# Kernel optimization log

Measured on AMD Instinct MI355X. Metric: run time of the kernel, lower is better.

The kernel has to match this reference:

```python
import jax, jax.numpy as jnp
import numpy as np

N_USERS = 50000
N_ITEMS = 100000
N = N_USERS + N_ITEMS
D = 64
N_LAYERS = 3
N_INTENTS = 128
T_SIZE = 32
TEMP = 0.2
KL_REG = 0.01
EMB_REG = 1e-5
INT_REG = 1e-5
SSL_REG = 0.1
B = 4096
E_RAND = 3_000_000


def setup_inputs() -> dict:
    key = jax.random.key(0)
    ks = jax.random.split(key, 12)
    # edge list: random edges + self loops so every node has degree >= 1
    h_rand = jax.random.randint(ks[0], (E_RAND,), 0, N, dtype=jnp.int32)
    t_rand = jax.random.randint(ks[1], (E_RAND,), 0, N, dtype=jnp.int32)
    loops = jnp.arange(N, dtype=jnp.int32)
    h_list = jnp.concatenate([loops, h_rand])
    t_list = jnp.concatenate([loops, t_rand])
    return {
        "user_emb": jax.random.normal(ks[2], (N_USERS, D), jnp.float32) * 0.1,
        "item_emb": jax.random.normal(ks[3], (N_ITEMS, D), jnp.float32) * 0.1,
        "user_intent": jax.random.normal(ks[4], (D, N_INTENTS), jnp.float32) * 0.1,
        "item_intent": jax.random.normal(ks[5], (D, N_INTENTS), jnp.float32) * 0.1,
        "lin_w": jax.random.normal(ks[6], (D, T_SIZE), jnp.float32) * 0.1,
        "lin_b": jnp.zeros((D,), jnp.float32),
        "eps": jax.random.uniform(ks[7], (N, D), jnp.float32),
        "h_list": h_list,
        "t_list": t_list,
        "users": jax.random.randint(ks[8], (B,), 0, N_USERS, dtype=jnp.int32),
        "pos_items": jax.random.randint(ks[9], (B,), 0, N_ITEMS, dtype=jnp.int32),
        "neg_items": jax.random.randint(ks[10], (B,), 0, N_ITEMS, dtype=jnp.int32),
    }


def _normalize(x):
    return x / jnp.linalg.norm(x, axis=1, keepdims=True)


def _infonce(e1, e2):
    pos = jnp.exp(jnp.sum(e1 * e2, axis=1) / TEMP)                 # [B]
    neg = jnp.sum(jnp.exp(e1 @ e2.T / TEMP), axis=1)               # [B]
    return jnp.mean(-jnp.log(pos / (neg + 1e-8) + 1e-8))


def reference(user_emb, item_emb, user_intent, item_intent, lin_w, lin_b,
              eps, h_list, t_list, users, pos_items, neg_items):
    # ---- symmetric normalization D^-1/2 A D^-1/2 (A values = 1) ----
    deg = jax.ops.segment_sum(jnp.ones_like(h_list, dtype=jnp.float32), h_list,
                              num_segments=N)
    d_inv = deg ** -0.5
    g_vals = d_inv[h_list] * d_inv[t_list]                          # [E]

    # ---- multi-layer SpMM propagation, layer-sum aggregation ----
    ego = jnp.concatenate([user_emb, item_emb], axis=0)             # [N, D]
    acc = ego
    cur = ego
    for _ in range(N_LAYERS):
        cur = jax.ops.segment_sum(g_vals[:, None] * cur[t_list], h_list,
                                  num_segments=N)                   # spmm
        acc = acc + cur
    all_emb = acc                                                   # [N, D]
    ua, ia = all_emb[:N_USERS], all_emb[N_USERS:]

    # ---- generative learning ----
    mean = all_emb
    std = jax.nn.softplus(all_emb[:, :T_SIZE])
    std = std @ lin_w.T + lin_b + 1e-8                              # [N, D]
    gen_emb = mean + eps * std

    # ---- intent model ----
    u_int = jax.nn.softmax(ua @ user_intent, axis=1) @ user_intent.T
    i_int = jax.nn.softmax(ia @ item_intent, axis=1) @ item_intent.T

    # ---- BPR loss ----
    u_e = ua[users]
    pos_scores = jnp.sum(u_e * ia[pos_items], axis=1)
    neg_scores = jnp.sum(u_e * ia[neg_items], axis=1)
    bpr_loss = jnp.mean(jax.nn.softplus(neg_scores - pos_scores))

    # ---- KL loss ----
    kl = -0.5 * (1.0 + 2.0 * std - jnp.square(mean) - jnp.exp(2.0 * std))
    kl = jnp.where(jnp.isfinite(kl), kl, 0.0)
    kl_loss = KL_REG * jnp.mean(jnp.sum(kl, axis=1))
    gen_loss = bpr_loss + kl_loss

    # ---- embedding / intent regularizers ----
    emb_loss = EMB_REG * (jnp.sum(jnp.square(user_emb[users]))
                          + jnp.sum(jnp.square(item_emb[pos_items]))
                          + jnp.sum(jnp.square(item_emb[neg_items])))
    int_loss = INT_REG * (jnp.sum(jnp.square(user_intent))
                          + jnp.sum(jnp.square(item_intent)))

    # ---- SSL (InfoNCE) loss ----
    u_gen = _normalize(gen_emb[:N_USERS][users])
    i_gen = _normalize(gen_emb[N_USERS:][pos_items])
    u_i = _normalize(u_int[users])
    i_i = _normalize(i_int[pos_items])
    cl_loss = SSL_REG * (_infonce(u_gen, u_i) + _infonce(i_gen, i_i))

    return (gen_loss, cl_loss, emb_loss, int_loss)
```

## Files before the change

### kernel.cpp

```cpp
#include <hip/hip_runtime.h>

#define NU 50000
#define NI 100000
#define NT 150000
#define BB 4096
#define NBUCK 147
#define BCAP 24576
#define NCH 8

typedef __attribute__((ext_vector_type(8))) short bf16x8;
typedef __attribute__((ext_vector_type(4))) float f32x4;
typedef __attribute__((ext_vector_type(2))) float f32x2;
typedef unsigned long long u64;

__device__ __forceinline__ float softplusf(float x) {
  return fmaxf(x, 0.f) + __logf(1.f + __expf(-fabsf(x)));
}
__device__ __forceinline__ float wsum(float v) {
#pragma unroll
  for (int o = 32; o > 0; o >>= 1) v += __shfl_xor(v, o, 64);
  return v;
}
__device__ __forceinline__ unsigned short f2b(float x) {
  unsigned u = __float_as_uint(x);
  return (unsigned short)((u + 0x7FFFu + ((u >> 16) & 1u)) >> 16);
}
__device__ __forceinline__ float b2f(unsigned us) {
  return __uint_as_float(us << 16);
}
__device__ __forceinline__ float bfe(bf16x8 v, int j) {
  return __uint_as_float(((unsigned)(unsigned short)v[j]) << 16);
}
__device__ __forceinline__ void unp4(u64 v, float* o) {
  unsigned lo = (unsigned)v, hi = (unsigned)(v >> 32);
  o[0] = __uint_as_float(lo << 16);
  o[1] = __uint_as_float(lo & 0xffff0000u);
  o[2] = __uint_as_float(hi << 16);
  o[3] = __uint_as_float(hi & 0xffff0000u);
}
__device__ __forceinline__ u64 pk4(float x0, float x1, float x2, float x3) {
  return (u64)((unsigned)f2b(x0) | ((unsigned)f2b(x1) << 16)) |
         ((u64)((unsigned)f2b(x2) | ((unsigned)f2b(x3) << 16)) << 32);
}

__global__ void k_zero(int* __restrict__ gcur, float* __restrict__ negu,
                       float* __restrict__ negi, double* __restrict__ accums) {
  int t = threadIdx.x;
  for (int i = t; i < NBUCK; i += 256) gcur[i] = 0;
  for (int i = t; i < BB; i += 256) { negu[i] = 0.f; negi[i] = 0.f; }
  if (t < 8) accums[t] = 0.0;
}

__global__ __launch_bounds__(256) void k_part(const int* __restrict__ h,
                                              const int* __restrict__ t,
                                              int* __restrict__ gcur,
                                              uint2* __restrict__ part, int E) {
  __shared__ int cnt[NBUCK];
  __shared__ int base[NBUCK];
  for (int b = threadIdx.x; b < NBUCK; b += 256) cnt[b] = 0;
  __syncthreads();
  int e0 = blockIdx.x * 4096 + threadIdx.x * 16;
  int nval = E - e0;
  nval = nval < 0 ? 0 : (nval > 16 ? 16 : nval);
  int hh[16], tt[16];
  if (nval == 16) {
    const int4* hp = (const int4*)(h + e0);
    const int4* tp = (const int4*)(t + e0);
#pragma unroll
    for (int j = 0; j < 4; j++) {
      int4 v = hp[j];
      hh[j * 4] = v.x; hh[j * 4 + 1] = v.y; hh[j * 4 + 2] = v.z; hh[j * 4 + 3] = v.w;
      int4 w = tp[j];
      tt[j * 4] = w.x; tt[j * 4 + 1] = w.y; tt[j * 4 + 2] = w.z; tt[j * 4 + 3] = w.w;
    }
  } else {
    for (int j = 0; j < nval; j++) { hh[j] = h[e0 + j]; tt[j] = t[e0 + j]; }
  }
  for (int j = 0; j < nval; j++) atomicAdd(&cnt[hh[j] >> 10], 1);
  __syncthreads();
  for (int b = threadIdx.x; b < NBUCK; b += 256) {
    int c = cnt[b];
    base[b] = c ? atomicAdd(&gcur[b], c) : 0;
    cnt[b] = 0;
  }
  __syncthreads();
  for (int j = 0; j < nval; j++) {
    int b = hh[j] >> 10;
    int r = atomicAdd(&cnt[b], 1);
    uint2 v; v.x = (unsigned)hh[j]; v.y = (unsigned)tt[j];
    part[(size_t)b * BCAP + base[b] + r] = v;
  }
}

__global__ __launch_bounds__(256) void k_count2(const uint2* __restrict__ part,
                                                const int* __restrict__ gcur,
                                                int* __restrict__ cnt_chunk) {
  __shared__ int hist[1024];
  int b = blockIdx.x, c = blockIdx.y, tid = threadIdx.x;
  for (int i = tid; i < 1024; i += 256) hist[i] = 0;
  __syncthreads();
  int m = gcur[b];
  int lo = (int)(((long long)m * c) >> 3);
  int hi = (int)(((long long)m * (c + 1)) >> 3);
  const uint2* pp = part + (size_t)b * BCAP;
  for (int i = lo + tid; i < hi; i += 256) atomicAdd(&hist[pp[i].x & 1023], 1);
  __syncthreads();
  for (int i = tid; i < 1024; i += 256)
    cnt_chunk[((((size_t)b << 10) + i) << 3) + c] = hist[i];
}

__global__ __launch_bounds__(256) void k_node(int* __restrict__ cnt_chunk,
                                              int* __restrict__ rloc_g,
                                              float* __restrict__ d_inv,
                                              int* __restrict__ btot) {
  __shared__ int sd[256];
  int b = blockIdx.x, tid = threadIdx.x;
  int n0 = b << 10;
  int pd[4];
  int s = 0;
#pragma unroll
  for (int j = 0; j < 4; j++) {
    int idx = tid * 4 + j;
    size_t base = ((size_t)(n0 + idx)) << 3;
    int run = 0;
#pragma unroll
// ... 106 lines not shown
  for (int i = s; i < e; i += 32) {
    int ia = i + (int)d;
    int ib = ia + 16;
    u64 ra = ep[ia < e ? ia : e - 1];
    u64 rb = ep[ib < e ? ib : e - 1];
    unsigned rax = (unsigned)ra;
    unsigned ray = (ia < e) ? (unsigned)(ra >> 32) : 0u;
    unsigned rbx = (unsigned)rb;
    unsigned rby = (ib < e) ? (unsigned)(rb >> 32) : 0u;
    unsigned iA0 = __shfl(rax, b4 + 0, 64); float gA0 = __uint_as_float(__shfl(ray, b4 + 0, 64));
    unsigned iA1 = __shfl(rax, b4 + 1, 64); float gA1 = __uint_as_float(__shfl(ray, b4 + 1, 64));
    unsigned iA2 = __shfl(rax, b4 + 2, 64); float gA2 = __uint_as_float(__shfl(ray, b4 + 2, 64));
    unsigned iA3 = __shfl(rax, b4 + 3, 64); float gA3 = __uint_as_float(__shfl(ray, b4 + 3, 64));
    unsigned vA0 = cur[(iA0 << 4) + d];
    unsigned vA1 = cur[(iA1 << 4) + d];
    unsigned vA2 = cur[(iA2 << 4) + d];
    unsigned vA3 = cur[(iA3 << 4) + d];
    unsigned iB0 = __shfl(rbx, b4 + 0, 64); float gB0 = __uint_as_float(__shfl(rby, b4 + 0, 64));
    unsigned iB1 = __shfl(rbx, b4 + 1, 64); float gB1 = __uint_as_float(__shfl(rby, b4 + 1, 64));
    unsigned iB2 = __shfl(rbx, b4 + 2, 64); float gB2 = __uint_as_float(__shfl(rby, b4 + 2, 64));
    unsigned iB3 = __shfl(rbx, b4 + 3, 64); float gB3 = __uint_as_float(__shfl(rby, b4 + 3, 64));
    unsigned vB0 = cur[(iB0 << 4) + d];
    unsigned vB1 = cur[(iB1 << 4) + d];
    unsigned vB2 = cur[(iB2 << 4) + d];
    unsigned vB3 = cur[(iB3 << 4) + d];
    f32x2 lo, hi;
    lo = __builtin_amdgcn_cvt_pk_f32_fp8(vA0, false);
    hi = __builtin_amdgcn_cvt_pk_f32_fp8(vA0, true);
    a0 = fmaf(gA0, lo.x, a0); a1 = fmaf(gA0, lo.y, a1);
    a2 = fmaf(gA0, hi.x, a2); a3 = fmaf(gA0, hi.y, a3);
    lo = __builtin_amdgcn_cvt_pk_f32_fp8(vA1, false);
    hi = __builtin_amdgcn_cvt_pk_f32_fp8(vA1, true);
    a0 = fmaf(gA1, lo.x, a0); a1 = fmaf(gA1, lo.y, a1);
    a2 = fmaf(gA1, hi.x, a2); a3 = fmaf(gA1, hi.y, a3);
    lo = __builtin_amdgcn_cvt_pk_f32_fp8(vA2, false);
    hi = __builtin_amdgcn_cvt_pk_f32_fp8(vA2, true);
    a0 = fmaf(gA2, lo.x, a0); a1 = fmaf(gA2, lo.y, a1);
    a2 = fmaf(gA2, hi.x, a2); a3 = fmaf(gA2, hi.y, a3);
    lo = __builtin_amdgcn_cvt_pk_f32_fp8(vA3, false);
    hi = __builtin_amdgcn_cvt_pk_f32_fp8(vA3, true);
    a0 = fmaf(gA3, lo.x, a0); a1 = fmaf(gA3, lo.y, a1);
    a2 = fmaf(gA3, hi.x, a2); a3 = fmaf(gA3, hi.y, a3);
    lo = __builtin_amdgcn_cvt_pk_f32_fp8(vB0, false);
    hi = __builtin_amdgcn_cvt_pk_f32_fp8(vB0, true);
    a0 = fmaf(gB0, lo.x, a0); a1 = fmaf(gB0, lo.y, a1);
    a2 = fmaf(gB0, hi.x, a2); a3 = fmaf(gB0, hi.y, a3);
    lo = __builtin_amdgcn_cvt_pk_f32_fp8(vB1, false);
    hi = __builtin_amdgcn_cvt_pk_f32_fp8(vB1, true);
    a0 = fmaf(gB1, lo.x, a0); a1 = fmaf(gB1, lo.y, a1);
    a2 = fmaf(gB1, hi.x, a2); a3 = fmaf(gB1, hi.y, a3);
    lo = __builtin_amdgcn_cvt_pk_f32_fp8(vB2, false);
    hi = __builtin_amdgcn_cvt_pk_f32_fp8(vB2, true);
    a0 = fmaf(gB2, lo.x, a0); a1 = fmaf(gB2, lo.y, a1);
    a2 = fmaf(gB2, hi.x, a2); a3 = fmaf(gB2, hi.y, a3);
    lo = __builtin_amdgcn_cvt_pk_f32_fp8(vB3, false);
    hi = __builtin_amdgcn_cvt_pk_f32_fp8(vB3, true);
    a0 = fmaf(gB3, lo.x, a0); a1 = fmaf(gB3, lo.y, a1);
    a2 = fmaf(gB3, hi.x, a2); a3 = fmaf(gB3, hi.y, a3);
  }
  a0 += __shfl_xor(a0, 16, 64);
  a1 += __shfl_xor(a1, 16, 64);
  a2 += __shfl_xor(a2, 16, 64);
  a3 += __shfl_xor(a3, 16, 64);
  a0 += __shfl_xor(a0, 32, 64);
  a1 += __shfl_xor(a1, 32, 64);
  a2 += __shfl_xor(a2, 32, 64);
  a3 += __shfl_xor(a3, 32, 64);
  unsigned ro = ((unsigned)node << 4) + d;
  if (g == 0) {
    u64 pv = acc64[ro];
    unsigned lo32 = (unsigned)pv, hi32 = (unsigned)(pv >> 32);
    float x0 = __uint_as_float(lo32 << 16) + a0;
    float x1 = __uint_as_float(lo32 & 0xffff0000u) + a1;
    float x2 = __uint_as_float(hi32 << 16) + a2;
    float x3 = __uint_as_float(hi32 & 0xffff0000u) + a3;
    acc64[ro] = pk4(x0, x1, x2, x3);
  } else if (g == 1 && !last) {
    int p = __builtin_amdgcn_cvt_pk_fp8_f32(a0, a1, 0, false);
    p = __builtin_amdgcn_cvt_pk_fp8_f32(a2, a3, p, true);
    nxt[ro] = (unsigned)p;
  }
}

__global__ __launch_bounds__(256) void k_post(
    const unsigned short* __restrict__ accB,
    const float* __restrict__ user_emb, const float* __restrict__ item_emb,
    const float* __restrict__ eps,
    const float* __restrict__ user_int, const float* __restrict__ item_int,
    const float* __restrict__ lin_w, const float* __restrict__ lin_b,
    const int* __restrict__ users, const int* __restrict__ pos_items,
    const int* __restrict__ neg_items,
    unsigned short* __restrict__ ugen_b, unsigned short* __restrict__ uio_b,
    unsigned short* __restrict__ igen_b, unsigned short* __restrict__ iio_b,
    float* __restrict__ posu, float* __restrict__ posi,
    double* __restrict__ accums) {
  __shared__ __align__(16) unsigned short sUIT[128 * 72];
  __shared__ __align__(16) unsigned short sUI[64 * 136];
  __shared__ __align__(16) unsigned short sP[4][16 * 136];
  __shared__ double red[8];
  int bid = blockIdx.x;
  int lane = threadIdx.x & 63;
  int wid = threadIdx.x >> 6;
  int n = lane & 15, q = lane >> 4;
  if (bid < 128) {
    int isI = bid >> 6;
    int i0 = ((bid & 63) << 6) + wid * 16;
    const float* intent = isI ? item_int : user_int;
    for (int i = threadIdx.x; i < 8192; i += 256) {
      int dd = i >> 7, kk = i & 127;
      unsigned short v = f2b(intent[i]);
      sUIT[kk * 72 + dd] = v;
      sUI[dd * 136 + kk] = v;
    }
    __syncthreads();
    unsigned short* myP = &sP[wid][0];
    int piN = pos_items[i0 + n];
    int rw = isI ? (NU + piN) : users[i0 + n];
    const unsigned short* arp = accB + (size_t)rw * 64;
    bf16x8 a0 = *(const bf16x8*)(arp + q * 8);
    bf16x8 a1 = *(const bf16x8*)(arp + 32 + q * 8);
    f32x4 c[8];
#pragma unroll
    for (int kt = 0; kt < 8; kt++) {
      const unsigned short* bp = &sUIT[(kt * 16 + n) * 72 + q * 8];
      bf16x8 b0 = *(const bf16x8*)bp;
      bf16x8 b1 = *(const bf16x8*)(bp + 32);
      f32x4 z = {0.f, 0.f, 0.f, 0.f};
      z = __builtin_amdgcn_mfma_f32_16x16x32_bf16(a0, b0, z, 0, 0, 0);
      c[kt] = __builtin_amdgcn_mfma_f32_16x16x32_bf16(a1, b1, z, 0, 0, 0);
    }
    float mx[4], tot[4];
#pragma unroll
    for (int r = 0; r < 4; r++) {
      float m = c[0][r];
#pragma unroll
      for (int kt = 1; kt < 8; kt++) m = fmaxf(m, c[kt][r]);
#pragma unroll
      for (int o = 1; o < 16; o <<= 1) m = fmaxf(m, __shfl_xor(m, o, 64));
      mx[r] = m;
    }
#pragma unroll
    for (int kt = 0; kt < 8; kt++)
#pragma unroll
      for (int r = 0; r < 4; r++) c[kt][r] = __expf(c[kt][r] - mx[r]);
#pragma unroll
    for (int r = 0; r < 4; r++) {
      float t = 0.f;
#pragma unroll
      for (int kt = 0; kt < 8; kt++) t += c[kt][r];
#pragma unroll
      for (int o = 1; o < 16; o <<= 1) t += __shfl_xor(t, o, 64);
      tot[r] = 1.f / t;
    }
#pragma unroll
    for (int kt = 0; kt < 8; kt++)
#pragma unroll
      for (int r = 0; r < 4; r++)
        myP[(q * 4 + r) * 136 + kt * 16 + n] = f2b(c[kt][r] * tot[r]);
    f32x4 s[4];
#pragma unroll
    for (int dt = 0; dt < 4; dt++) s[dt] = (f32x4){0.f, 0.f, 0.f, 0.f};
#pragma unroll
    for (int cc = 0; cc < 4; cc++) {
      bf16x8 pa = *(const bf16x8*)&myP[n * 136 + cc * 32 + q * 8];
#pragma unroll
      for (int dt = 0; dt < 4; dt++) {
        bf16x8 bb = *(const bf16x8*)&sUI[(dt * 16 + n) * 136 + cc * 32 + q * 8];
        s[dt] = __builtin_amdgcn_mfma_f32_16x16x32_bf16(pa, bb, s[dt], 0, 0, 0);
      }
    }
    float rin[4];
#pragma unroll
    for (int r = 0; r < 4; r++) {
      float t = 0.f;
#pragma unroll
      for (int dt = 0; dt < 4; dt++) t += s[dt][r] * s[dt][r];
#pragma unroll
      for (int o = 1; o < 16; o <<= 1) t += __shfl_xor(t, o, 64);
      rin[r] = 1.f / sqrtf(t);
    }
    float iov[4][4];
    unsigned short* iob = isI ? iio_b : uio_b;
#pragma unroll
    for (int dt = 0; dt < 4; dt++)
#pragma unroll
      for (int r = 0; r < 4; r++) {
        float v = s[dt][r] * rin[r];
        iov[dt][r] = v;
        iob[(size_t)(i0 + q * 4 + r) * 64 + dt * 16 + n] = f2b(v);
      }
    bf16x8 A3;
#pragma unroll
    for (int j = 0; j < 8; j++) A3[j] = (short)f2b(softplusf(bfe(a0, j)));
    f32x4 sd4[4];
    float lbv[4];
#pragma unroll
    for (int dt = 0; dt < 4; dt++) {
      const float* wp = lin_w + (size_t)(dt * 16 + n) * 32 + q * 8;
      float4 w0 = *(const float4*)wp;
      float4 w1 = *(const float4*)(wp + 4);
      bf16x8 B3;
      B3[0] = (short)f2b(w0.x); B3[1] = (short)f2b(w0.y);
      B3[2] = (short)f2b(w0.z); B3[3] = (short)f2b(w0.w);
      B3[4] = (short)f2b(w1.x); B3[5] = (short)f2b(w1.y);
      B3[6] = (short)f2b(w1.z); B3[7] = (short)f2b(w1.w);
      f32x4 z = {0.f, 0.f, 0.f, 0.f};
      sd4[dt] = __builtin_amdgcn_mfma_f32_16x16x32_bf16(A3, B3, z, 0, 0, 0);
      lbv[dt] = lin_b[dt * 16 + n];
    }
    *(bf16x8*)&myP[n * 136 + q * 8] = a0;
    *(bf16x8*)&myP[n * 136 + 32 + q * 8] = a1;
    int rwr[4];
#pragma unroll
    for (int r = 0; r < 4; r++) rwr[r] = __shfl(rw, q * 4 + r, 64);
    float ge[4][4];
#pragma unroll
    for (int dt = 0; dt < 4; dt++)
#pragma unroll
      for (int r = 0; r < 4; r++) {
        float mcv = b2f(myP[(q * 4 + r) * 136 + dt * 16 + n]);
        float ep = eps[(size_t)rwr[r] * 64 + dt * 16 + n];
        float sdf = sd4[dt][r] + lbv[dt] + 1e-8f;
        ge[dt][r] = mcv + ep * sdf;
      }
    float gin[4];
#pragma unroll
    for (int r = 0; r < 4; r++) {
      float t = 0.f;
#pragma unroll
      for (int dt = 0; dt < 4; dt++) t += ge[dt][r] * ge[dt][r];
#pragma unroll
      for (int o = 1; o < 16; o <<= 1) t += __shfl_xor(t, o, 64);
      gin[r] = 1.f / sqrtf(t);
    }
    float pd[4] = {0.f, 0.f, 0.f, 0.f};
    unsigned short* gob = isI ? igen_b : ugen_b;
#pragma unroll
    for (int dt = 0; dt < 4; dt++)
#pragma unroll
      for (int r = 0; r < 4; r++) {
        float go = ge[dt][r] * gin[r];
        gob[(size_t)(i0 + q * 4 + r) * 64 + dt * 16 + n] = f2b(go);
        pd[r] = fmaf(go, iov[dt][r], pd[r]);
      }
    float* posX = isI ? posi : posu;
#pragma unroll
    for (int r = 0; r < 4; r++) {
      float t = pd[r];
#pragma unroll
      for (int o = 1; o < 16; o <<= 1) t += __shfl_xor(t, o, 64);
      if (n == 0) posX[i0 + q * 4 + r] = t;
    }
    if (!isI) {
      int niN = neg_items[i0 + n];
      const unsigned short* pp = accB + (size_t)(NU + piN) * 64;
      const unsigned short* np = accB + (size_t)(NU + niN) * 64;
      bf16x8 p0 = *(const bf16x8*)(pp + q * 8);
      bf16x8 p1 = *(const bf16x8*)(pp + 32 + q * 8);
      bf16x8 n0 = *(const bf16x8*)(np + q * 8);
      bf16x8 n1 = *(const bf16x8*)(np + 32 + q * 8);
      float ps = 0.f, ns = 0.f;
#pragma unroll
      for (int j = 0; j < 8; j++) {
        float m0 = bfe(a0, j), m1 = bfe(a1, j);
        ps = fmaf(m0, bfe(p0, j), ps); ps = fmaf(m1, bfe(p1, j), ps);
        ns = fmaf(m0, bfe(n0, j), ns); ns = fmaf(m1, bfe(n1, j), ns);
      }
      ps += __shfl_xor(ps, 16, 64); ps += __shfl_xor(ps, 32, 64);
      ns += __shfl_xor(ns, 16, 64); ns += __shfl_xor(ns, 32, 64);
      float bpr = softplusf(ns - ps);
      const float* uep = user_emb + (size_t)rw * 64 + q * 16;
      float es = 0.f;
#pragma unroll
      for (int j = 0; j < 4; j++) {
        float4 u4 = *(const float4*)(uep + j * 4);
        es += u4.x * u4.x + u4.y * u4.y + u4.z * u4.z + u4.w * u4.w;
      }
      es += __shfl_xor(es, 16, 64); es += __shfl_xor(es, 32, 64);
#pragma unroll
      for (int o = 1; o < 16; o <<= 1) {
        bpr += __shfl_xor(bpr, o, 64);
        es += __shfl_xor(es, o, 64);
      }
      if (lane == 0) { red[wid] = (double)bpr; red[4 + wid] = (double)es; }
      __syncthreads();
      if (threadIdx.x == 0) {
        atomicAdd(&accums[0], red[0] + red[1] + red[2] + red[3]);
        atomicAdd(&accums[2], red[4] + red[5] + red[6] + red[7]);
      }
    } else {
      int niN = neg_items[i0 + n];
      const float* pe = item_emb + (size_t)piN * 64 + q * 16;
      const float* ne = item_emb + (size_t)niN * 64 + q * 16;
      float es = 0.f;
#pragma unroll
      for (int j = 0; j < 4; j++) {
        float4 u4 = *(const float4*)(pe + j * 4);
        float4 v4 = *(const float4*)(ne + j * 4);
        es += u4.x * u4.x + u4.y * u4.y + u4.z * u4.z + u4.w * u4.w;
        es += v4.x * v4.x + v4.y * v4.y + v4.z * v4.z + v4.w * v4.w;
      }
      es += __shfl_xor(es, 16, 64); es += __shfl_xor(es, 32, 64);
#pragma unroll
      for (int o = 1; o < 16; o <<= 1) es += __shfl_xor(es, o, 64);
      if (lane == 0) red[wid] = (double)es;
      __syncthreads();
      if (threadIdx.x == 0)
        atomicAdd(&accums[2], red[0] + red[1] + red[2] + red[3]);
    }
  } else if (bid < 128 + 1920) {
    bf16x8 B0, B1, B2, B3;
    float lb0, lb1, lb2, lb3;
    {
      const float* w0 = lin_w + (0 * 16 + n) * 32 + q * 8;
      const float* w1 = lin_w + (1 * 16 + n) * 32 + q * 8;
      const float* w2 = lin_w + (2 * 16 + n) * 32 + q * 8;
      const float* w3 = lin_w + (3 * 16 + n) * 32 + q * 8;
#pragma unroll
      for (int j = 0; j < 8; j++) {
        B0[j] = (short)f2b(w0[j]);
        B1[j] = (short)f2b(w1[j]);
        B2[j] = (short)f2b(w2[j]);
        B3[j] = (short)f2b(w3[j]);
      }
      lb0 = lin_b[0 * 16 + n] + 1e-8f;
      lb1 = lin_b[1 * 16 + n] + 1e-8f;
      lb2 = lin_b[2 * 16 + n] + 1e-8f;
      lb3 = lin_b[3 * 16 + n] + 1e-8f;
    }
    const int TI = NT / 16;
    int w0id = (bid - 128) * 4 + wid;
    int nwv = 1920 * 4;
    double dsum = 0.0;
    for (int tile = w0id; tile < TI; tile += nwv) {
      const u64* rp = (const u64*)(accB + (size_t)(tile * 16 + n) * 64 + q * 8);
      u64 A0 = rp[0];
      u64 A1 = rp[1];
      u64 C0 = rp[8];
      u64 C1 = rp[9];
      float av[8], bv[8];
      unp4(A0, av); unp4(A1, av + 4);
      unp4(C0, bv); unp4(C1, bv + 4);
      float msum = 0.f;
#pragma unroll
      for (int j = 0; j < 8; j++) msum += av[j] * av[j] + bv[j] * bv[j];
      bf16x8 Af;
#pragma unroll
      for (int j = 0; j < 8; j++) Af[j] = (short)f2b(softplusf(av[j]));
      f32x4 z = {0.f, 0.f, 0.f, 0.f};
      f32x4 c0 = __builtin_amdgcn_mfma_f32_16x16x32_bf16(Af, B0, z, 0, 0, 0);
      f32x4 c1 = __builtin_amdgcn_mfma_f32_16x16x32_bf16(Af, B1, z, 0, 0, 0);
      f32x4 c2 = __builtin_amdgcn_mfma_f32_16x16x32_bf16(Af, B2, z, 0, 0, 0);
      f32x4 c3 = __builtin_amdgcn_mfma_f32_16x16x32_bf16(Af, B3, z, 0, 0, 0);
      float ksum = 0.f;
#pragma unroll
      for (int r = 0; r < 4; r++) {
        float s0 = c0[r] + lb0, s1 = c1[r] + lb1, s2 = c2[r] + lb2, s3 = c3[r] + lb3;
        ksum += -0.5f * (1.f + 2.f * s0 - __expf(2.f * s0));
        ksum += -0.5f * (1.f + 2.f * s1 - __expf(2.f * s1));
        ksum += -0.5f * (1.f + 2.f * s2 - __expf(2.f * s2));
        ksum += -0.5f * (1.f + 2.f * s3 - __expf(2.f * s3));
      }
      dsum += (double)wsum(ksum + 0.5f * msum);
    }
    if (lane == 0) red[wid] = dsum;
    __syncthreads();
    if (threadIdx.x == 0)
      atomicAdd(&accums[1], red[0] + red[1] + red[2] + red[3]);
  } else {
    float s = 0.f;
    for (int i = threadIdx.x; i < 64 * 128; i += 256) {
      float a = user_int[i], b = item_int[i];
      s = fmaf(a, a, s);
      s = fmaf(b, b, s);
    }
    s = wsum(s);
    if (lane == 0) red[wid] = (double)s;
    __syncthreads();
    if (threadIdx.x == 0)
      atomicAdd(&accums[3], red[0] + red[1] + red[2] + red[3]);
  }
}

__global__ __launch_bounds__(256) void k_nce(
    const unsigned short* __restrict__ e1u, const unsigned short* __restrict__ e2u,
    const unsigned short* __restrict__ e1i, const unsigned short* __restrict__ e2i,
    float* __restrict__ negu, float* __restrict__ negi) {
  int pr = blockIdx.y >> 4, jq = blockIdx.y & 15;
  const unsigned short* e1 = pr ? e1i : e1u;
  const unsigned short* e2 = pr ? e2i : e2u;
  float* nego = pr ? negi : negu;
  int wid = threadIdx.x >> 6, lane = threadIdx.x & 63;
  int q = lane >> 4, n = lane & 15;
  int i0 = blockIdx.x * 64 + wid * 16;
  const bf16x8* arow = (const bf16x8*)(e1 + (size_t)(i0 + n) * 64 + q * 8);
  bf16x8 a0 = arow[0];
  bf16x8 a1 = arow[4];
  f32x4 accv = {0.f, 0.f, 0.f, 0.f};
  int j0 = jq * 256;
  for (int jt = 0; jt < 16; jt += 2) {
    const bf16x8* br0 = (const bf16x8*)(e2 + (size_t)(j0 + jt * 16 + n) * 64 + q * 8);
    const bf16x8* br1 = (const bf16x8*)(e2 + (size_t)(j0 + (jt + 1) * 16 + n) * 64 + q * 8);
    bf16x8 b0 = br0[0];
    bf16x8 b1 = br0[4];
    bf16x8 b2 = br1[0];
    bf16x8 b3 = br1[4];
    f32x4 c = {0.f, 0.f, 0.f, 0.f};
    f32x4 c2 = {0.f, 0.f, 0.f, 0.f};
    c = __builtin_amdgcn_mfma_f32_16x16x32_bf16(a0, b0, c, 0, 0, 0);
    c = __builtin_amdgcn_mfma_f32_16x16x32_bf16(a1, b1, c, 0, 0, 0);
    c2 = __builtin_amdgcn_mfma_f32_16x16x32_bf16(a0, b2, c2, 0, 0, 0);
    c2 = __builtin_amdgcn_mfma_f32_16x16x32_bf16(a1, b3, c2, 0, 0, 0);
#pragma unroll
    for (int r = 0; r < 4; r++)
      accv[r] += __expf(5.0f * c[r]) + __expf(5.0f * c2[r]);
  }
#pragma unroll
  for (int o = 1; o < 16; o <<= 1) {
#pragma unroll
    for (int r = 0; r < 4; r++) accv[r] += __shfl_xor(accv[r], o, 64);
  }
  if (n == 0) {
#pragma unroll
    for (int r = 0; r < 4; r++) atomicAdd(&nego[i0 + q * 4 + r], accv[r]);
  }
}

__global__ __launch_bounds__(256) void k_out(
    const float* __restrict__ posu, const float* __restrict__ posi,
    const float* __restrict__ negu, const float* __restrict__ negi,
    const double* __restrict__ accums, float* __restrict__ out) {
  __shared__ double redd[4];
  double cl = 0.0;
  for (int i = threadIdx.x; i < 2 * BB; i += 256) {
    int pr = i >> 12, idx = i & (BB - 1);
    float ng = pr ? negi[idx] : negu[idx];
    float dt = pr ? posi[idx] : posu[idx];
    float pos = expf(5.0f * dt);
    cl += (double)(-logf(pos / (ng + 1e-8f) + 1e-8f));
  }
#pragma unroll
  for (int o = 32; o > 0; o >>= 1) cl += __shfl_xor(cl, o, 64);
  int lane = threadIdx.x & 63, wid = threadIdx.x >> 6;
  if (lane == 0) redd[wid] = cl;
  __syncthreads();
  if (threadIdx.x == 0) {
    double cls = redd[0] + redd[1] + redd[2] + redd[3];
    double bpr = accums[0] / (double)BB;
    double kl = 0.01 * accums[1] / (double)NT;
    out[0] = (float)(bpr + kl);
    out[1] = (float)(0.1 * cls / (double)BB);
    out[2] = (float)(1e-5 * accums[2]);
    out[3] = (float)(1e-5 * accums[3]);
  }
}

extern "C" void kernel_launch(void* const* d_in, const int* in_sizes, int n_in,
                              void* d_out, int out_size, void* d_ws, size_t ws_size,
                              hipStream_t stream) {
  const float* user_emb = (const float*)d_in[0];
  const float* item_emb = (const float*)d_in[1];
  const float* user_int = (const float*)d_in[2];
  const float* item_int = (const float*)d_in[3];
  const float* lin_w = (const float*)d_in[4];
  const float* lin_b = (const float*)d_in[5];
  const float* eps = (const float*)d_in[6];
  const int* h_list = (const int*)d_in[7];
  const int* t_list = (const int*)d_in[8];
  const int* users = (const int*)d_in[9];
  const int* pos_items = (const int*)d_in[10];
  const int* neg_items = (const int*)d_in[11];
  float* out = (float*)d_out;
  const int E = in_sizes[7];

  char* ws = (char*)d_ws;
  size_t off = 0;
  auto take = [&](size_t bytes) -> char* {
    char* p = ws + off;
    off = (off + bytes + 255) & ~(size_t)255;
    return p;
  };
  int* row_ptr = (int*)take((size_t)(NT + 1) * 4);
  float* d_inv = (float*)take((size_t)NT * 4);
  int* rloc_g = (int*)take((size_t)NT * 4);
  int* cnt_chunk = (int*)take((size_t)NBUCK * NCH * 1024 * 4);
  int* gcur = (int*)take(NBUCK * 4);
  int* btot = (int*)take(NBUCK * 4);
  uint2* edges = (uint2*)take((size_t)E * 8);
  unsigned* bufA = (unsigned*)take((size_t)NT * 16 * 4);
  unsigned* bufB = (unsigned*)take((size_t)NT * 16 * 4);
  unsigned short* accB = (unsigned short*)take((size_t)NBUCK * BCAP * 8);
  unsigned short* ugen_b = (unsigned short*)take((size_t)BB * 64 * 2);
  unsigned short* igen_b = (unsigned short*)take((size_t)BB * 64 * 2);
  unsigned short* uio_b = (unsigned short*)take((size_t)BB * 64 * 2);
  unsigned short* iio_b = (unsigned short*)take((size_t)BB * 64 * 2);
  float* posu = (float*)take((size_t)BB * 4);
  float* posi = (float*)take((size_t)BB * 4);
  float* negu = (float*)take((size_t)BB * 4);
  float* negi = (float*)take((size_t)BB * 4);
  double* accums = (double*)take(64);
  if (off > ws_size) return;
  uint2* part = (uint2*)accB;
  u64* acc64 = (u64*)accB;

  k_zero<<<1, 256, 0, stream>>>(gcur, negu, negi, accums);

  int gridP = (E + 4095) / 4096;
  k_part<<<gridP, 256, 0, stream>>>(h_list, t_list, gcur, part, E);
  k_count2<<<dim3(NBUCK, NCH), 256, 0, stream>>>(part, gcur, cnt_chunk);
  k_node<<<NBUCK, 256, 0, stream>>>(cnt_chunk, rloc_g, d_inv, btot);
  k_fill2<<<dim3(NBUCK, NCH), 256, 0, stream>>>(part, gcur, cnt_chunk, rloc_g,
                                                btot, d_inv, edges, row_ptr);

  int nU4 = NU * 16, nTot4 = NT * 16;
  k_init<<<(nTot4 + 255) / 256, 256, 0, stream>>>((const float4*)user_emb,
                                                  (const float4*)item_emb, bufA,
                                                  acc64, nU4, nTot4);
  int gridAgg = NT / 4;
  k_agg<<<gridAgg, 256, 0, stream>>>(row_ptr, edges, bufA, bufB, acc64, 0);
  k_agg<<<gridAgg, 256, 0, stream>>>(row_ptr, edges, bufB, bufA, acc64, 0);
  k_agg<<<gridAgg, 256, 0, stream>>>(row_ptr, edges, bufA, bufB, acc64, 1);

  k_post<<<128 + 1920 + 1, 256, 0, stream>>>(accB, user_emb, item_emb, eps,
                                             user_int, item_int, lin_w, lin_b,
                                             users, pos_items, neg_items,
                                             ugen_b, uio_b, igen_b, iio_b,
                                             posu, posi, accums);
  k_nce<<<dim3(64, 32), 256, 0, stream>>>(ugen_b, uio_b, igen_b, iio_b,
                                          negu, negi);
  k_out<<<1, 256, 0, stream>>>(posu, posi, negu, negi, accums, out);
}
```

Baseline: 461.2 us.

## Split batch work into own kernel and co-schedule KL pass with InfoNCE

```diff
diff --git a/kernel.cpp b/kernel.cpp
--- a/kernel.cpp
+++ b/kernel.cpp
@@ -39,8 +39,10 @@
   o[3] = __uint_as_float(hi & 0xffff0000u);
 }
 __device__ __forceinline__ u64 pk4(float x0, float x1, float x2, float x3) {
-  return (u64)((unsigned)f2b(x0) | ((unsigned)f2b(x1) << 16)) |
-         ((u64)((unsigned)f2b(x2) | ((unsigned)f2b(x3) << 16)) << 32);
+  unsigned lo, hi;
+  asm("v_cvt_pk_bf16_f32 %0, %1, %2" : "=v"(lo) : "v"(x0), "v"(x1));
+  asm("v_cvt_pk_bf16_f32 %0, %1, %2" : "=v"(hi) : "v"(x2), "v"(x3));
+  return ((u64)hi << 32) | lo;
 }
 
 __global__ void k_zero(int* __restrict__ gcur, float* __restrict__ negu,
@@ -313,7 +315,7 @@
   }
 }
 
-__global__ __launch_bounds__(256) void k_post(
+__global__ __launch_bounds__(256) void k_batch(
     const unsigned short* __restrict__ accB,
     const float* __restrict__ user_emb, const float* __restrict__ item_emb,
     const float* __restrict__ eps,
@@ -333,213 +335,265 @@
   int lane = threadIdx.x & 63;
   int wid = threadIdx.x >> 6;
   int n = lane & 15, q = lane >> 4;
-  if (bid < 128) {
-    int isI = bid >> 6;
-    int i0 = ((bid & 63) << 6) + wid * 16;
-    const float* intent = isI ? item_int : user_int;
-    for (int i = threadIdx.x; i < 8192; i += 256) {
-      int dd = i >> 7, kk = i & 127;
-      unsigned short v = f2b(intent[i]);
-      sUIT[kk * 72 + dd] = v;
-      sUI[dd * 136 + kk] = v;
-    }
+  int isI = bid >> 6;
+  int i0 = ((bid & 63) << 6) + wid * 16;
+  const float* intent = isI ? item_int : user_int;
+  for (int i = threadIdx.x; i < 8192; i += 256) {
+    int dd = i >> 7, kk = i & 127;
+    unsigned short v = f2b(intent[i]);
+    sUIT[kk * 72 + dd] = v;
+    sUI[dd * 136 + kk] = v;
+  }
+  __syncthreads();
+  unsigned short* myP = &sP[wid][0];
+  int piN = pos_items[i0 + n];
+  int rw = isI ? (NU + piN) : users[i0 + n];
+  const unsigned short* arp = accB + (size_t)rw * 64;
+  bf16x8 a0 = *(const bf16x8*)(arp + q * 8);
+  bf16x8 a1 = *(const bf16x8*)(arp + 32 + q * 8);
+  f32x4 c[8];
+#pragma unroll
+  for (int kt = 0; kt < 8; kt++) {
+    const unsigned short* bp = &sUIT[(kt * 16 + n) * 72 + q * 8];
+    bf16x8 b0 = *(const bf16x8*)bp;
+    bf16x8 b1 = *(const bf16x8*)(bp + 32);
+    f32x4 z = {0.f, 0.f, 0.f, 0.f};
+    z = __builtin_amdgcn_mfma_f32_16x16x32_bf16(a0, b0, z, 0, 0, 0);
+    c[kt] = __builtin_amdgcn_mfma_f32_16x16x32_bf16(a1, b1, z, 0, 0, 0);
+  }
+  float mx[4], tot[4];
+#pragma unroll
+  for (int r = 0; r < 4; r++) {
+    float m = c[0][r];
+#pragma unroll
+    for (int kt = 1; kt < 8; kt++) m = fmaxf(m, c[kt][r]);
+#pragma unroll
+    for (int o = 1; o < 16; o <<= 1) m = fmaxf(m, __shfl_xor(m, o, 64));
+    mx[r] = m;
+  }
+#pragma unroll
+  for (int kt = 0; kt < 8; kt++)
+#pragma unroll
+    for (int r = 0; r < 4; r++) c[kt][r] = __expf(c[kt][r] - mx[r]);
+#pragma unroll
+  for (int r = 0; r < 4; r++) {
+    float t = 0.f;
+#pragma unroll
+    for (int kt = 0; kt < 8; kt++) t += c[kt][r];
+#pragma unroll
+    for (int o = 1; o < 16; o <<= 1) t += __shfl_xor(t, o, 64);
+    tot[r] = 1.f / t;
+  }
+#pragma unroll
+  for (int kt = 0; kt < 8; kt++)
+#pragma unroll
+    for (int r = 0; r < 4; r++)
+      myP[(q * 4 + r) * 136 + kt * 16 + n] = f2b(c[kt][r] * tot[r]);
+  f32x4 s[4];
+#pragma unroll
+  for (int dt = 0; dt < 4; dt++) s[dt] = (f32x4){0.f, 0.f, 0.f, 0.f};
+#pragma unroll
+  for (int cc = 0; cc < 4; cc++) {
+    bf16x8 pa = *(const bf16x8*)&myP[n * 136 + cc * 32 + q * 8];
+#pragma unroll
+    for (int dt = 0; dt < 4; dt++) {
+      bf16x8 bb = *(const bf16x8*)&sUI[(dt * 16 + n) * 136 + cc * 32 + q * 8];
+      s[dt] = __builtin_amdgcn_mfma_f32_16x16x32_bf16(pa, bb, s[dt], 0, 0, 0);
+    }
+  }
+  float rin[4];
+#pragma unroll
+  for (int r = 0; r < 4; r++) {
+    float t = 0.f;
+#pragma unroll
+    for (int dt = 0; dt < 4; dt++) t += s[dt][r] * s[dt][r];
+#pragma unroll
+    for (int o = 1; o < 16; o <<= 1) t += __shfl_xor(t, o, 64);
+    rin[r] = 1.f / sqrtf(t);
+  }
+  float iov[4][4];
+  unsigned short* iob = isI ? iio_b : uio_b;
+#pragma unroll
+  for (int dt = 0; dt < 4; dt++)
+#pragma unroll
+    for (int r = 0; r < 4; r++) {
+      float v = s[dt][r] * rin[r];
+      iov[dt][r] = v;
+      iob[(size_t)(i0 + q * 4 + r) * 64 + dt * 16 + n] = f2b(v);
+    }
+  bf16x8 A3;
+#pragma unroll
+  for (int j = 0; j < 8; j++) A3[j] = (short)f2b(softplusf(bfe(a0, j)));
+  f32x4 sd4[4];
+  float lbv[4];
+#pragma unroll
+  for (int dt = 0; dt < 4; dt++) {
+    const float* wp = lin_w + (size_t)(dt * 16 + n) * 32 + q * 8;
+    float4 w0 = *(const float4*)wp;
+    float4 w1 = *(const float4*)(wp + 4);
+    bf16x8 B3;
+    B3[0] = (short)f2b(w0.x); B3[1] = (short)f2b(w0.y);
+    B3[2] = (short)f2b(w0.z); B3[3] = (short)f2b(w0.w);
+    B3[4] = (short)f2b(w1.x); B3[5] = (short)f2b(w1.y);
+    B3[6] = (short)f2b(w1.z); B3[7] = (short)f2b(w1.w);
+    f32x4 z = {0.f, 0.f, 0.f, 0.f};
+    sd4[dt] = __builtin_amdgcn_mfma_f32_16x16x32_bf16(A3, B3, z, 0, 0, 0);
+    lbv[dt] = lin_b[dt * 16 + n];
+  }
+  *(bf16x8*)&myP[n * 136 + q * 8] = a0;
+  *(bf16x8*)&myP[n * 136 + 32 + q * 8] = a1;
+  int rwr[4];
+#pragma unroll
+  for (int r = 0; r < 4; r++) rwr[r] = __shfl(rw, q * 4 + r, 64);
+  float ge[4][4];
+#pragma unroll
+  for (int dt = 0; dt < 4; dt++)
+#pragma unroll
+    for (int r = 0; r < 4; r++) {
+      float mcv = b2f(myP[(q * 4 + r) * 136 + dt * 16 + n]);
+      float ep = eps[(size_t)rwr[r] * 64 + dt * 16 + n];
+      float sdf = sd4[dt][r] + lbv[dt] + 1e-8f;
+      ge[dt][r] = mcv + ep * sdf;
+    }
+  float gin[4];
+#pragma unroll
+  for (int r = 0; r < 4; r++) {
+    float t = 0.f;
+#pragma unroll
+    for (int dt = 0; dt < 4; dt++) t += ge[dt][r] * ge[dt][r];
+#pragma unroll
+    for (int o = 1; o < 16; o <<= 1) t += __shfl_xor(t, o, 64);
+    gin[r] = 1.f / sqrtf(t);
+  }
+  float pd[4] = {0.f, 0.f, 0.f, 0.f};
+  unsigned short* gob = isI ? igen_b : ugen_b;
+#pragma unroll
+  for (int dt = 0; dt < 4; dt++)
+#pragma unroll
+    for (int r = 0; r < 4; r++) {
+      float go = ge[dt][r] * gin[r];
+      gob[(size_t)(i0 + q * 4 + r) * 64 + dt * 16 + n] = f2b(go);
+      pd[r] = fmaf(go, iov[dt][r], pd[r]);
+    }
+  float* posX = isI ? posi : posu;
+#pragma unroll
+  for (int r = 0; r < 4; r++) {
+    float t = pd[r];
+#pragma unroll
+    for (int o = 1; o < 16; o <<= 1) t += __shfl_xor(t, o, 64);
+    if (n == 0) posX[i0 + q * 4 + r] = t;
+  }
+  if (!isI) {
+    int niN = neg_items[i0 + n];
+    const unsigned short* pp = accB + (size_t)(NU + piN) * 64;
+    const unsigned short* np = accB + (size_t)(NU + niN) * 64;
+    bf16x8 p0 = *(const bf16x8*)(pp + q * 8);
+    bf16x8 p1 = *(const bf16x8*)(pp + 32 + q * 8);
+    bf16x8 n0 = *(const bf16x8*)(np + q * 8);
+    bf16x8 n1 = *(const bf16x8*)(np + 32 + q * 8);
+    float ps = 0.f, ns = 0.f;
+#pragma unroll
+    for (int j = 0; j < 8; j++) {
+      float m0 = bfe(a0, j), m1 = bfe(a1, j);
+      ps = fmaf(m0, bfe(p0, j), ps); ps = fmaf(m1, bfe(p1, j), ps);
+      ns = fmaf(m0, bfe(n0, j), ns); ns = fmaf(m1, bfe(n1, j), ns);
+    }
+    ps += __shfl_xor(ps, 16, 64); ps += __shfl_xor(ps, 32, 64);
+    ns += __shfl_xor(ns, 16, 64); ns += __shfl_xor(ns, 32, 64);
+    float bpr = softplusf(ns - ps);
+    const float* uep = user_emb + (size_t)rw * 64 + q * 16;
+    float es = 0.f;
+#pragma unroll
+    for (int j = 0; j < 4; j++) {
+      float4 u4 = *(const float4*)(uep + j * 4);
+      es += u4.x * u4.x + u4.y * u4.y + u4.z * u4.z + u4.w * u4.w;
+    }
+    es += __shfl_xor(es, 16, 64); es += __shfl_xor(es, 32, 64);
+#pragma unroll
+    for (int o = 1; o < 16; o <<= 1) {
+      bpr += __shfl_xor(bpr, o, 64);
+      es += __shfl_xor(es, o, 64);
+    }
+    if (lane == 0) { red[wid] = (double)bpr; red[4 + wid] = (double)es; }
     __syncthreads();
-    unsigned short* myP = &sP[wid][0];
-    int piN = pos_items[i0 + n];
-    int rw = isI ? (NU + piN) : users[i0 + n];
-    const unsigned short* arp = accB + (size_t)rw * 64;
-    bf16x8 a0 = *(const bf16x8*)(arp + q * 8);
-    bf16x8 a1 = *(const bf16x8*)(arp + 32 + q * 8);
-    f32x4 c[8];
-#pragma unroll
-    for (int kt = 0; kt < 8; kt++) {
-      const unsigned short* bp = &sUIT[(kt * 16 + n) * 72 + q * 8];
-      bf16x8 b0 = *(const bf16x8*)bp;
-      bf16x8 b1 = *(const bf16x8*)(bp + 32);
-      f32x4 z = {0.f, 0.f, 0.f, 0.f};
-      z = __builtin_amdgcn_mfma_f32_16x16x32_bf16(a0, b0, z, 0, 0, 0);
-      c[kt] = __builtin_amdgcn_mfma_f32_16x16x32_bf16(a1, b1, z, 0, 0, 0);
-    }
-    float mx[4], tot[4];
-#pragma unroll
-    for (int r = 0; r < 4; r++) {
-      float m = c[0][r];
-#pragma unroll
-      for (int kt = 1; kt < 8; kt++) m = fmaxf(m, c[kt][r]);
-#pragma unroll
-      for (int o = 1; o < 16; o <<= 1) m = fmaxf(m, __shfl_xor(m, o, 64));
-      mx[r] = m;
-    }
-#pragma unroll
-    for (int kt = 0; kt < 8; kt++)
-#pragma unroll
-      for (int r = 0; r < 4; r++) c[kt][r] = __expf(c[kt][r] - mx[r]);
-#pragma unroll
-    for (int r = 0; r < 4; r++) {
-      float t = 0.f;
-#pragma unroll
-      for (int kt = 0; kt < 8; kt++) t += c[kt][r];
-#pragma unroll
-      for (int o = 1; o < 16; o <<= 1) t += __shfl_xor(t, o, 64);
-      tot[r] = 1.f / t;
-    }
-#pragma unroll
-    for (int kt = 0; kt < 8; kt++)
+    if (threadIdx.x == 0) {
+      atomicAdd(&accums[0], red[0] + red[1] + red[2] + red[3]);
+      atomicAdd(&accums[2], red[4] + red[5] + red[6] + red[7]);
+    }
+  } else {
+    int niN = neg_items[i0 + n];
+    const float* pe = item_emb + (size_t)piN * 64 + q * 16;
+    const float* ne = item_emb + (size_t)niN * 64 + q * 16;
+    float es = 0.f;
+#pragma unroll
+    for (int j = 0; j < 4; j++) {
+      float4 u4 = *(const float4*)(pe + j * 4);
+      float4 v4 = *(const float4*)(ne + j * 4);
+      es += u4.x * u4.x + u4.y * u4.y + u4.z * u4.z + u4.w * u4.w;
+      es += v4.x * v4.x + v4.y * v4.y + v4.z * v4.z + v4.w * v4.w;
+    }
+    es += __shfl_xor(es, 16, 64); es += __shfl_xor(es, 32, 64);
+#pragma unroll
+    for (int o = 1; o < 16; o <<= 1) es += __shfl_xor(es, o, 64);
+    if (lane == 0) red[wid] = (double)es;
+    __syncthreads();
+    if (threadIdx.x == 0)
+      atomicAdd(&accums[2], red[0] + red[1] + red[2] + red[3]);
+  }
+}
+
+__global__ __launch_bounds__(256) void k_nk(
+    const unsigned short* __restrict__ e1u, const unsigned short* __restrict__ e2u,
+    const unsigned short* __restrict__ e1i, const unsigned short* __restrict__ e2i,
+    float* __restrict__ negu, float* __restrict__ negi,
+    const unsigned short* __restrict__ accB,
+    const float* __restrict__ lin_w, const float* __restrict__ lin_b,
+    const float* __restrict__ user_int, const float* __restrict__ item_int,
+    double* __restrict__ accums) {
+  __shared__ double red[8];
+  int bid = blockIdx.x;
+  int lane = threadIdx.x & 63;
+  int wid = threadIdx.x >> 6;
+  int n = lane & 15, q = lane >> 4;
+  if (bid < 2048) {
+    int bx = bid & 63, by = bid >> 6;
+    int pr = by >> 4, jq = by & 15;
+    const unsigned short* e1 = pr ? e1i : e1u;
+    const unsigned short* e2 = pr ? e2i : e2u;
+    float* nego = pr ? negi : negu;
+    int i0 = bx * 64 + wid * 16;
+    const bf16x8* arow = (const bf16x8*)(e1 + (size_t)(i0 + n) * 64 + q * 8);
+    bf16x8 a0 = arow[0];
+    bf16x8 a1 = arow[4];
+    f32x4 accv = {0.f, 0.f, 0.f, 0.f};
+    int j0 = jq * 256;
+    for (int jt = 0; jt < 16; jt += 2) {
+      const bf16x8* br0 = (const bf16x8*)(e2 + (size_t)(j0 + jt * 16 + n) * 64 + q * 8);
+      const bf16x8* br1 = (const bf16x8*)(e2 + (size_t)(j0 + (jt + 1) * 16 + n) * 64 + q * 8);
+      bf16x8 b0 = br0[0];
+      bf16x8 b1 = br0[4];
+      bf16x8 b2 = br1[0];
+      bf16x8 b3 = br1[4];
+      f32x4 c = {0.f, 0.f, 0.f, 0.f};
+      f32x4 c2 = {0.f, 0.f, 0.f, 0.f};
+      c = __builtin_amdgcn_mfma_f32_16x16x32_bf16(a0, b0, c, 0, 0, 0);
+      c = __builtin_amdgcn_mfma_f32_16x16x32_bf16(a1, b1, c, 0, 0, 0);
+      c2 = __builtin_amdgcn_mfma_f32_16x16x32_bf16(a0, b2, c2, 0, 0, 0);
+      c2 = __builtin_amdgcn_mfma_f32_16x16x32_bf16(a1, b3, c2, 0, 0, 0);
 #pragma unroll
       for (int r = 0; r < 4; r++)
-        myP[(q * 4 + r) * 136 + kt * 16 + n] = f2b(c[kt][r] * tot[r]);
-    f32x4 s[4];
-#pragma unroll
-    for (int dt = 0; dt < 4; dt++) s[dt] = (f32x4){0.f, 0.f, 0.f, 0.f};
-#pragma unroll
-    for (int cc = 0; cc < 4; cc++) {
-      bf16x8 pa = *(const bf16x8*)&myP[n * 136 + cc * 32 + q * 8];
-#pragma unroll
-      for (int dt = 0; dt < 4; dt++) {
-        bf16x8 bb = *(const bf16x8*)&sUI[(dt * 16 + n) * 136 + cc * 32 + q * 8];
-        s[dt] = __builtin_amdgcn_mfma_f32_16x16x32_bf16(pa, bb, s[dt], 0, 0, 0);
-      }
-    }
-    float rin[4];
-#pragma unroll
-    for (int r = 0; r < 4; r++) {
-      float t = 0.f;
-#pragma unroll
-      for (int dt = 0; dt < 4; dt++) t += s[dt][r] * s[dt][r];
-#pragma unroll
-      for (int o = 1; o < 16; o <<= 1) t += __shfl_xor(t, o, 64);
-      rin[r] = 1.f / sqrtf(t);
-    }
-    float iov[4][4];
-    unsigned short* iob = isI ? iio_b : uio_b;
-#pragma unroll
-    for (int dt = 0; dt < 4; dt++)
-#pragma unroll
-      for (int r = 0; r < 4; r++) {
-        float v = s[dt][r] * rin[r];
-        iov[dt][r] = v;
-        iob[(size_t)(i0 + q * 4 + r) * 64 + dt * 16 + n] = f2b(v);
-      }
-    bf16x8 A3;
-#pragma unroll
-    for (int j = 0; j < 8; j++) A3[j] = (short)f2b(softplusf(bfe(a0, j)));
-    f32x4 sd4[4];
-    float lbv[4];
-#pragma unroll
-    for (int dt = 0; dt < 4; dt++) {
-      const float* wp = lin_w + (size_t)(dt * 16 + n) * 32 + q * 8;
-      float4 w0 = *(const float4*)wp;
-      float4 w1 = *(const float4*)(wp + 4);
-      bf16x8 B3;
-      B3[0] = (short)f2b(w0.x); B3[1] = (short)f2b(w0.y);
-      B3[2] = (short)f2b(w0.z); B3[3] = (short)f2b(w0.w);
-      B3[4] = (short)f2b(w1.x); B3[5] = (short)f2b(w1.y);
-      B3[6] = (short)f2b(w1.z); B3[7] = (short)f2b(w1.w);
-      f32x4 z = {0.f, 0.f, 0.f, 0.f};
-      sd4[dt] = __builtin_amdgcn_mfma_f32_16x16x32_bf16(A3, B3, z, 0, 0, 0);
-      lbv[dt] = lin_b[dt * 16 + n];
-    }
-    *(bf16x8*)&myP[n * 136 + q * 8] = a0;
-    *(bf16x8*)&myP[n * 136 + 32 + q * 8] = a1;
-    int rwr[4];
-#pragma unroll
-    for (int r = 0; r < 4; r++) rwr[r] = __shfl(rw, q * 4 + r, 64);
-    float ge[4][4];
-#pragma unroll
-    for (int dt = 0; dt < 4; dt++)
-#pragma unroll
-      for (int r = 0; r < 4; r++) {
-        float mcv = b2f(myP[(q * 4 + r) * 136 + dt * 16 + n]);
-        float ep = eps[(size_t)rwr[r] * 64 + dt * 16 + n];
-        float sdf = sd4[dt][r] + lbv[dt] + 1e-8f;
-        ge[dt][r] = mcv + ep * sdf;
-      }
-    float gin[4];
-#pragma unroll
-    for (int r = 0; r < 4; r++) {
-      float t = 0.f;
-#pragma unroll
-      for (int dt = 0; dt < 4; dt++) t += ge[dt][r] * ge[dt][r];
-#pragma unroll
-      for (int o = 1; o < 16; o <<= 1) t += __shfl_xor(t, o, 64);
-      gin[r] = 1.f / sqrtf(t);
-    }
-    float pd[4] = {0.f, 0.f, 0.f, 0.f};
-    unsigned short* gob = isI ? igen_b : ugen_b;
-#pragma unroll
-    for (int dt = 0; dt < 4; dt++)
-#pragma unroll
-      for (int r = 0; r < 4; r++) {
-        float go = ge[dt][r] * gin[r];
-        gob[(size_t)(i0 + q * 4 + r) * 64 + dt * 16 + n] = f2b(go);
-        pd[r] = fmaf(go, iov[dt][r], pd[r]);
-      }
-    float* posX = isI ? posi : posu;
-#pragma unroll
-    for (int r = 0; r < 4; r++) {
-      float t = pd[r];
-#pragma unroll
-      for (int o = 1; o < 16; o <<= 1) t += __shfl_xor(t, o, 64);
-      if (n == 0) posX[i0 + q * 4 + r] = t;
-    }
-    if (!isI) {
-      int niN = neg_items[i0 + n];
-      const unsigned short* pp = accB + (size_t)(NU + piN) * 64;
-      const unsigned short* np = accB + (size_t)(NU + niN) * 64;
-      bf16x8 p0 = *(const bf16x8*)(pp + q * 8);
-      bf16x8 p1 = *(const bf16x8*)(pp + 32 + q * 8);
-      bf16x8 n0 = *(const bf16x8*)(np + q * 8);
-      bf16x8 n1 = *(const bf16x8*)(np + 32 + q * 8);
-      float ps = 0.f, ns = 0.f;
-#pragma unroll
-      for (int j = 0; j < 8; j++) {
-        float m0 = bfe(a0, j), m1 = bfe(a1, j);
-        ps = fmaf(m0, bfe(p0, j), ps); ps = fmaf(m1, bfe(p1, j), ps);
-        ns = fmaf(m0, bfe(n0, j), ns); ns = fmaf(m1, bfe(n1, j), ns);
-      }
-      ps += __shfl_xor(ps, 16, 64); ps += __shfl_xor(ps, 32, 64);
-      ns += __shfl_xor(ns, 16, 64); ns += __shfl_xor(ns, 32, 64);
-      float bpr = softplusf(ns - ps);
-      const float* uep = user_emb + (size_t)rw * 64 + q * 16;
-      float es = 0.f;
-#pragma unroll
-      for (int j = 0; j < 4; j++) {
-        float4 u4 = *(const float4*)(uep + j * 4);
-        es += u4.x * u4.x + u4.y * u4.y + u4.z * u4.z + u4.w * u4.w;
-      }
-      es += __shfl_xor(es, 16, 64); es += __shfl_xor(es, 32, 64);
-#pragma unroll
-      for (int o = 1; o < 16; o <<= 1) {
-        bpr += __shfl_xor(bpr, o, 64);
-        es += __shfl_xor(es, o, 64);
-      }
-      if (lane == 0) { red[wid] = (double)bpr; red[4 + wid] = (double)es; }
-      __syncthreads();
-      if (threadIdx.x == 0) {
-        atomicAdd(&accums[0], red[0] + red[1] + red[2] + red[3]);
-        atomicAdd(&accums[2], red[4] + red[5] + red[6] + red[7]);
-      }
-    } else {
-      int niN = neg_items[i0 + n];
-      const float* pe = item_emb + (size_t)piN * 64 + q * 16;
-      const float* ne = item_emb + (size_t)niN * 64 + q * 16;
-      float es = 0.f;
-#pragma unroll
-      for (int j = 0; j < 4; j++) {
-        float4 u4 = *(const float4*)(pe + j * 4);
-        float4 v4 = *(const float4*)(ne + j * 4);
-        es += u4.x * u4.x + u4.y * u4.y + u4.z * u4.z + u4.w * u4.w;
-        es += v4.x * v4.x + v4.y * v4.y + v4.z * v4.z + v4.w * v4.w;
-      }
-      es += __shfl_xor(es, 16, 64); es += __shfl_xor(es, 32, 64);
-#pragma unroll
-      for (int o = 1; o < 16; o <<= 1) es += __shfl_xor(es, o, 64);
-      if (lane == 0) red[wid] = (double)es;
-      __syncthreads();
-      if (threadIdx.x == 0)
-        atomicAdd(&accums[2], red[0] + red[1] + red[2] + red[3]);
-    }
-  } else if (bid < 128 + 1920) {
+        accv[r] += __expf(5.0f * c[r]) + __expf(5.0f * c2[r]);
+    }
+#pragma unroll
+    for (int o = 1; o < 16; o <<= 1) {
+#pragma unroll
+      for (int r = 0; r < 4; r++) accv[r] += __shfl_xor(accv[r], o, 64);
+    }
+    if (n == 0) {
+#pragma unroll
+      for (int r = 0; r < 4; r++) atomicAdd(&nego[i0 + q * 4 + r], accv[r]);
+    }
+  } else if (bid < 2048 + 1920) {
     bf16x8 B0, B1, B2, B3;
     float lb0, lb1, lb2, lb3;
     {
@@ -560,7 +614,7 @@
       lb3 = lin_b[3 * 16 + n] + 1e-8f;
     }
     const int TI = NT / 16;
-    int w0id = (bid - 128) * 4 + wid;
+    int w0id = (bid - 2048) * 4 + wid;
     int nwv = 1920 * 4;
     double dsum = 0.0;
     for (int tile = w0id; tile < TI; tile += nwv) {
@@ -610,50 +664,6 @@
     __syncthreads();
     if (threadIdx.x == 0)
       atomicAdd(&accums[3], red[0] + red[1] + red[2] + red[3]);
-  }
-}
-
-__global__ __launch_bounds__(256) void k_nce(
-    const unsigned short* __restrict__ e1u, const unsigned short* __restrict__ e2u,
-    const unsigned short* __restrict__ e1i, const unsigned short* __restrict__ e2i,
-    float* __restrict__ negu, float* __restrict__ negi) {
-  int pr = blockIdx.y >> 4, jq = blockIdx.y & 15;
-  const unsigned short* e1 = pr ? e1i : e1u;
-  const unsigned short* e2 = pr ? e2i : e2u;
-  float* nego = pr ? negi : negu;
-  int wid = threadIdx.x >> 6, lane = threadIdx.x & 63;
-  int q = lane >> 4, n = lane & 15;
-  int i0 = blockIdx.x * 64 + wid * 16;
-  const bf16x8* arow = (const bf16x8*)(e1 + (size_t)(i0 + n) * 64 + q * 8);
-  bf16x8 a0 = arow[0];
-  bf16x8 a1 = arow[4];
-  f32x4 accv = {0.f, 0.f, 0.f, 0.f};
-  int j0 = jq * 256;
-  for (int jt = 0; jt < 16; jt += 2) {
-    const bf16x8* br0 = (const bf16x8*)(e2 + (size_t)(j0 + jt * 16 + n) * 64 + q * 8);
-    const bf16x8* br1 = (const bf16x8*)(e2 + (size_t)(j0 + (jt + 1) * 16 + n) * 64 + q * 8);
-    bf16x8 b0 = br0[0];
-    bf16x8 b1 = br0[4];
-    bf16x8 b2 = br1[0];
-    bf16x8 b3 = br1[4];
-    f32x4 c = {0.f, 0.f, 0.f, 0.f};
-    f32x4 c2 = {0.f, 0.f, 0.f, 0.f};
-    c = __builtin_amdgcn_mfma_f32_16x16x32_bf16(a0, b0, c, 0, 0, 0);
-    c = __builtin_amdgcn_mfma_f32_16x16x32_bf16(a1, b1, c, 0, 0, 0);
-    c2 = __builtin_amdgcn_mfma_f32_16x16x32_bf16(a0, b2, c2, 0, 0, 0);
-    c2 = __builtin_amdgcn_mfma_f32_16x16x32_bf16(a1, b3, c2, 0, 0, 0);
-#pragma unroll
-    for (int r = 0; r < 4; r++)
-      accv[r] += __expf(5.0f * c[r]) + __expf(5.0f * c2[r]);
-  }
-#pragma unroll
-  for (int o = 1; o < 16; o <<= 1) {
-#pragma unroll
-    for (int r = 0; r < 4; r++) accv[r] += __shfl_xor(accv[r], o, 64);
-  }
-  if (n == 0) {
-#pragma unroll
-    for (int r = 0; r < 4; r++) atomicAdd(&nego[i0 + q * 4 + r], accv[r]);
   }
 }
 
@@ -752,12 +762,13 @@
   k_agg<<<gridAgg, 256, 0, stream>>>(row_ptr, edges, bufB, bufA, acc64, 0);
   k_agg<<<gridAgg, 256, 0, stream>>>(row_ptr, edges, bufA, bufB, acc64, 1);
 
-  k_post<<<128 + 1920 + 1, 256, 0, stream>>>(accB, user_emb, item_emb, eps,
-                                             user_int, item_int, lin_w, lin_b,
-                                             users, pos_items, neg_items,
-                                             ugen_b, uio_b, igen_b, iio_b,
-                                             posu, posi, accums);
-  k_nce<<<dim3(64, 32), 256, 0, stream>>>(ugen_b, uio_b, igen_b, iio_b,
-                                          negu, negi);
+  k_batch<<<128, 256, 0, stream>>>(accB, user_emb, item_emb, eps,
+                                   user_int, item_int, lin_w, lin_b,
+                                   users, pos_items, neg_items,
+                                   ugen_b, uio_b, igen_b, iio_b,
+                                   posu, posi, accums);
+  k_nk<<<2048 + 1920 + 1, 256, 0, stream>>>(ugen_b, uio_b, igen_b, iio_b,
+                                            negu, negi, accB, lin_w, lin_b,
+                                            user_int, item_int, accums);
   k_out<<<1, 256, 0, stream>>>(posu, posi, negu, negi, accums, out);
 }
```

Result: slower. 471.2 us (+2.2%).
